# Kernel tuning notes

Measured on AMD Instinct MI355X. Metric: run time of the kernel, lower is better.

The kernel has to match this reference:

```python
import jax, jax.numpy as jnp
import numpy as np

HIDDEN = 2048
N_HEADS = 32
N_KV_HEADS = 8
HEAD_DIM = 64
MAX_SEQ_LEN = 4096
ROPE_THETA = 500000.0
B, L = 1, 2048
EPS = 1e-6
NEG = -1e9


def precompute_rope(head_dim, max_seq_len, theta):
    freqs = 1.0 / theta ** (jnp.arange(0, head_dim, 2, dtype=jnp.float32) / head_dim)
    pos = jnp.arange(max_seq_len, dtype=jnp.float32)
    ang = pos[:, None] * freqs[None, :]                     # [S, hd/2]
    cos = jnp.repeat(jnp.cos(ang), 2, axis=-1)              # [S, hd]
    sin = jnp.repeat(jnp.sin(ang), 2, axis=-1)
    return cos, sin


def apply_rope(x, cos, sin):
    # x: [B, H, L, hd]; interleaved (even/odd) rotation, faithful to torch code
    seq_len = x.shape[2]
    c = cos[:seq_len][None, None, :, ::2]                   # [1,1,L,hd/2]
    s = sin[:seq_len][None, None, :, ::2]
    x1 = x[..., ::2]
    x2 = x[..., 1::2]
    o1 = x1 * c - x2 * s
    o2 = x2 * c + x1 * s
    return jnp.stack([o1, o2], axis=-1).reshape(x.shape)


def rmsnorm(x, w):
    return x * jax.lax.rsqrt(jnp.mean(x * x, axis=-1, keepdims=True) + EPS) * w


def setup_inputs() -> dict:
    key = jax.random.key(0)
    ks = jax.random.split(key, 6)
    x = jax.random.normal(ks[0], (B, L, HIDDEN), dtype=jnp.float32)
    causal = jnp.tril(jnp.ones((L, L), dtype=bool))
    mask = jnp.where(causal, 0.0, NEG).astype(jnp.float32)  # additive causal mask
    scale = 0.02
    norm_w = jnp.ones((HIDDEN,), dtype=jnp.float32)
    Wq = jax.random.normal(ks[1], (N_HEADS * HEAD_DIM, HIDDEN), dtype=jnp.float32) * scale
    Wk = jax.random.normal(ks[2], (N_KV_HEADS * HEAD_DIM, HIDDEN), dtype=jnp.float32) * scale
    Wv = jax.random.normal(ks[3], (N_KV_HEADS * HEAD_DIM, HIDDEN), dtype=jnp.float32) * scale
    Wo = jax.random.normal(ks[4], (HIDDEN, N_HEADS * HEAD_DIM), dtype=jnp.float32) * scale
    rope_cos, rope_sin = precompute_rope(HEAD_DIM, MAX_SEQ_LEN, ROPE_THETA)
    return {"x": x, "mask": mask, "norm_w": norm_w, "Wq": Wq, "Wk": Wk,
            "Wv": Wv, "Wo": Wo, "rope_cos": rope_cos, "rope_sin": rope_sin}


def reference(x, mask, norm_w, Wq, Wk, Wv, Wo, rope_cos, rope_sin):
    Bb, Ll, _ = x.shape
    residual = x
    h = rmsnorm(x, norm_w)
    q = (h @ Wq.T).reshape(Bb, Ll, N_HEADS, HEAD_DIM).transpose(0, 2, 1, 3)     # [B,H,L,hd]
    k = (h @ Wk.T).reshape(Bb, Ll, N_KV_HEADS, HEAD_DIM).transpose(0, 2, 1, 3)  # [B,Hk,L,hd]
    v = (h @ Wv.T).reshape(Bb, Ll, N_KV_HEADS, HEAD_DIM).transpose(0, 2, 1, 3)
    q = apply_rope(q, rope_cos, rope_sin)
    k = apply_rope(k, rope_cos, rope_sin)
    n_groups = N_HEADS // N_KV_HEADS
    if n_groups > 1:
        k = jnp.repeat(k, n_groups, axis=1)   # GQA repeat_interleave
        v = jnp.repeat(v, n_groups, axis=1)
    scale = jnp.sqrt(jnp.asarray(HEAD_DIM, dtype=q.dtype))
    attn = jnp.einsum('bhld,bhmd->bhlm', q, k) / scale
    attn = attn + mask                                       # broadcast [L,L]
    attn = jax.nn.softmax(attn, axis=-1)
    out = jnp.einsum('bhlm,bhmd->bhld', attn, v)
    out = out.transpose(0, 2, 1, 3).reshape(Bb, Ll, N_HEADS * HEAD_DIM)
    return out @ Wo.T + residual
```

## Files before the change

kernel.cpp:

```cpp
#include <hip/hip_runtime.h>
#include <stdint.h>

#define L_SEQ 2048
#define HID   2048
#define NHEAD 32
#define NKV   8
#define HD    64
#define KVDIM 512
#define QSCALE 0.18033688f

typedef __attribute__((ext_vector_type(8))) short s16x8;
typedef __attribute__((ext_vector_type(4))) short s16x4;
typedef __attribute__((ext_vector_type(4))) float f32x4;

__device__ __forceinline__ short f2bf(float f) {
  __bf16 b = (__bf16)f;
  short s;
  __builtin_memcpy(&s, &b, 2);
  return s;
}

__device__ __forceinline__ void gload16(const void* g, void* l) {
  __builtin_amdgcn_global_load_lds(
      (const __attribute__((address_space(1))) void*)g,
      (__attribute__((address_space(3))) void*)l, 16, 0, 0);
}

__global__ __launch_bounds__(256) void pre_kernel(
    const float* __restrict__ x, const float* __restrict__ w,
    const float* __restrict__ wq, const float* __restrict__ wk,
    const float* __restrict__ wv, const float* __restrict__ wo,
    short* __restrict__ h,
    short* __restrict__ owq, short* __restrict__ owk,
    short* __restrict__ owv, short* __restrict__ owo) {
  const int tid = threadIdx.x;
  if (blockIdx.x >= 2048) {
    int64_t e = ((int64_t)(blockIdx.x - 2048) * 256 + tid) * 4;
    const float* src; short* dst; int64_t o;
    if (e < 4194304)      { src = wq; dst = owq; o = e; }
    else if (e < 5242880) { src = wk; dst = owk; o = e - 4194304; }
    else if (e < 6291456) { src = wv; dst = owv; o = e - 5242880; }
    else                  { src = wo; dst = owo; o = e - 6291456; }
    f32x4 v = *(const f32x4*)(src + o);
    s16x4 b;
    b[0] = f2bf(v[0]); b[1] = f2bf(v[1]); b[2] = f2bf(v[2]); b[3] = f2bf(v[3]);
    *(s16x4*)(dst + o) = b;
    return;
  }
  const int row = blockIdx.x;
  const float* xr = x + (int64_t)row * HID + tid * 8;
  f32x4 a = *(const f32x4*)(xr);
  f32x4 b = *(const f32x4*)(xr + 4);
  float ss = a[0]*a[0]+a[1]*a[1]+a[2]*a[2]+a[3]*a[3]
           + b[0]*b[0]+b[1]*b[1]+b[2]*b[2]+b[3]*b[3];
  #pragma unroll
  for (int off = 1; off < 64; off <<= 1) ss += __shfl_xor(ss, off, 64);
  __shared__ float sred[4];
  if ((tid & 63) == 0) sred[tid >> 6] = ss;
  __syncthreads();
  const float scale = rsqrtf((sred[0]+sred[1]+sred[2]+sred[3]) * (1.0f/HID) + 1e-6f);
  const float* wp = w + tid * 8;
  f32x4 wa = *(const f32x4*)(wp);
  f32x4 wb = *(const f32x4*)(wp + 4);
  s16x8 o;
  o[0]=f2bf(a[0]*scale*wa[0]); o[1]=f2bf(a[1]*scale*wa[1]);
  o[2]=f2bf(a[2]*scale*wa[2]); o[3]=f2bf(a[3]*scale*wa[3]);
  o[4]=f2bf(b[0]*scale*wb[0]); o[5]=f2bf(b[1]*scale*wb[1]);
  o[6]=f2bf(b[2]*scale*wb[2]); o[7]=f2bf(b[3]*scale*wb[3]);
  *(s16x8*)(h + (int64_t)row * HID + tid * 8) = o;
}

__device__ __forceinline__ void gemm_core_128x64(
    const short* __restrict__ A, const short* __restrict__ B,
    short* sA, short* sB, f32x4 acc[4][2]) {
  const int tid = threadIdx.x;
  const int lane = tid & 63;
  const int w = tid >> 6, wr = w >> 1, wc = w & 1;
  const int g = lane >> 4, li = lane & 15;

  auto stage = [&](int k0, int buf) {
    #pragma unroll
    for (int i = 0; i < 4; ++i) {
      const int flat = i * 256 + tid;
      const int row = flat >> 3, c8 = flat & 7;
      const int sc = c8 ^ (row & 7);
      gload16(A + (int64_t)row * HID + k0 + sc * 8, sA + buf * 8192 + flat * 8);
    }
    #pragma unroll
    for (int i = 0; i < 2; ++i) {
      const int flat = i * 256 + tid;
      const int row = flat >> 3, c8 = flat & 7;
      const int sc = c8 ^ (row & 7);
      gload16(B + (int64_t)row * HID + k0 + sc * 8, sB + buf * 4096 + flat * 8);
    }
  };

  stage(0, 0);
  for (int k0 = 0; k0 < HID; k0 += 64) {
    const int cur = (k0 >> 6) & 1;
    __syncthreads();
    if (k0 + 64 < HID) stage(k0 + 64, cur ^ 1);
    const short* cA = sA + cur * 8192;
    const short* cB = sB + cur * 4096;
    #pragma unroll
    for (int kk = 0; kk < 2; ++kk) {
      s16x8 af[4], bfr[2];
      const int chunk = (kk << 2) | g;
      #pragma unroll
      for (int m = 0; m < 4; ++m) {
        const int row = wr * 64 + m * 16 + li;
        af[m] = *(const s16x8*)(cA + row * 64 + ((chunk ^ (li & 7)) << 3));
      }
      #pragma unroll
      for (int n = 0; n < 2; ++n) {
        const int row = wc * 32 + n * 16 + li;
        bfr[n] = *(const s16x8*)(cB + row * 64 + ((chunk ^ (li & 7)) << 3));
      }
      __builtin_amdgcn_s_setprio(1);
      #pragma unroll
      for (int m = 0; m < 4; ++m)
        #pragma unroll
        for (int n = 0; n < 2; ++n)
          acc[m][n] = __builtin_amdgcn_mfma_f32_16x16x32_bf16(af[m], bfr[n], acc[m][n], 0, 0, 0);
      __builtin_amdgcn_s_setprio(0);
    }
  }
}

__global__ __launch_bounds__(256) void qkv_kernel(
    const short* __restrict__ h16, const short* __restrict__ wq,
    const short* __restrict__ wk, const short* __restrict__ wv,
    short* __restrict__ qo, short* __restrict__ ko, short* __restrict__ vto,
    const float* __restrict__ rc, const float* __restrict__ rs) {
  __shared__ short sA[2 * 128 * 64];
  __shared__ short sB[2 * 64 * 64];
  const int cb = blockIdx.x, rb = blockIdx.y;
  const short* B; short* out; int colbase, mode; int64_t ldc;
  if (cb < 32)      { B = wq + (int64_t)cb * 64 * HID;        out = qo;  colbase = cb * 64;        mode = 0; ldc = HID;   }
  else if (cb < 40) { B = wk + (int64_t)(cb - 32) * 64 * HID; out = ko;  colbase = (cb - 32) * 64; mode = 0; ldc = KVDIM; }
  else              { B = wv + (int64_t)(cb - 40) * 64 * HID; out = vto; colbase = (cb - 40) * 64; mode = 1; ldc = L_SEQ; }
  const float rsc = (cb < 32) ? QSCALE : 1.0f;

  f32x4 acc[4][2];
  const f32x4 z = {0.f, 0.f, 0.f, 0.f};
  #pragma unroll
  for (int m = 0; m < 4; ++m)
    #pragma unroll
    for (int n = 0; n < 2; ++n) acc[m][n] = z;

  gemm_core_128x64(h16 + (int64_t)rb * 128 * HID, B, sA, sB, acc);

  const int lane = threadIdx.x & 63;
  const int w = threadIdx.x >> 6, wr = w >> 1, wc = w & 1;
  const int g = lane >> 4, li = lane & 15;

  if (mode == 0) {
    #pragma unroll
    for (int m = 0; m < 4; ++m) {
      #pragma unroll
      for (int n = 0; n < 2; ++n) {
        const int col = colbase + wc * 32 + n * 16 + li;
        const int d2 = col & 62;
        #pragma unroll
        for (int r = 0; r < 4; ++r) {
          const int row = rb * 128 + wr * 64 + m * 16 + g * 4 + r;
          const float c = rc[row * 64 + d2] * rsc;
          const float s = rs[row * 64 + d2] * rsc;
          const float v0 = acc[m][n][r];
          const float pr = __shfl_xor(v0, 1, 64);
          const float o = (lane & 1) ? (v0 * c + pr * s) : (v0 * c - pr * s);
          out[(int64_t)row * ldc + col] = f2bf(o);
        }
      }
    }
  } else {
    #pragma unroll
    for (int m = 0; m < 4; ++m) {
      #pragma unroll
      for (int n = 0; n < 2; ++n) {
        const int col = colbase + wc * 32 + n * 16 + li;
        const int row0 = rb * 128 + wr * 64 + m * 16 + g * 4;
        s16x4 pk;
        pk[0] = f2bf(acc[m][n][0]); pk[1] = f2bf(acc[m][n][1]);
        pk[2] = f2bf(acc[m][n][2]); pk[3] = f2bf(acc[m][n][3]);
        *(s16x4*)(out + (int64_t)col * L_SEQ + row0) = pk;
      }
    }
  }
}

__global__ __launch_bounds__(512, 4) void attn_kernel(
    const short* __restrict__ q16, const short* __restrict__ k16,
    const short* __restrict__ vt16, short* __restrict__ out16) {
  __shared__ short sK[4 * 64 * 64];
  __shared__ short sV[4 * 64 * 64];
  __shared__ short sP[8][16 * 64];
  const int pi = blockIdx.x, h = blockIdx.y, kvh = h >> 2;
  const int qbL = pi, qbH = 31 - pi;
  const int tid = threadIdx.x, lane = tid & 63, w = tid >> 6, wl = w & 3;
  const int g = lane >> 4, li = lane & 15;
  const int myqb = (w < 4) ? qbL : qbH;
  short* sPw = &sP[w][0];

  s16x8 qf[2];
  {
    const int qr = myqb * 64 + wl * 16 + li;
    #pragma unroll
    for (int kk = 0; kk < 2; ++kk)
      qf[kk] = *(const s16x8*)(q16 + (int64_t)qr * HID + h * 64 + kk * 32 + g * 8);
  }

  f32x4 acc[4];
  const f32x4 z = {0.f, 0.f, 0.f, 0.f};
  #pragma unroll
  for (int n = 0; n < 4; ++n) acc[n] = z;
  float m = -1e30f, l = 0.f;

  auto stage1 = [&](int t, int buf, int slot) {
    const int kv0 = t * 64;
    const int row = tid >> 3, c8 = tid & 7;
    const int sc = c8 ^ (row & 7);
    const int off = (buf * 2 + slot) * 4096;
    gload16(k16 + (int64_t)(kv0 + row) * KVDIM + kvh * 64 + sc * 8,
            sK + off + tid * 8);
    gload16(vt16 + (int64_t)(kvh * 64 + row) * L_SEQ + kv0 + sc * 8,
            sV + off + tid * 8);
  };

  stage1(0, 0, 0);
  stage1(1, 0, 1);
  for (int tp = 0; 2 * tp <= qbH; ++tp) {
    const int buf = tp & 1;
    __syncthreads();
    if (2 * tp + 2 <= qbH) {
      stage1(2 * tp + 2, buf ^ 1, 0);
      const int t3 = 2 * tp + 3;
      stage1(t3 <= qbH ? t3 : t3 - 1, buf ^ 1, 1);
    }
    #pragma unroll
    for (int sl = 0; sl < 2; ++sl) {
      const int t = 2 * tp + sl;
      if (t <= qbH && (w >= 4 || t <= qbL)) {
        const short* cK = sK + (buf * 2 + sl) * 4096;
        const short* cV = sV + (buf * 2 + sl) * 4096;

        s16x8 kf[2][4];
        #pragma unroll
        for (int kk = 0; kk < 2; ++kk)
          #pragma unroll
          for (int n = 0; n < 4; ++n)
            kf[kk][n] = *(const s16x8*)(cK + (n * 16 + li) * 64 + ((((kk << 2) | g) ^ (li & 7)) << 3));
        f32x4 s[4];
        #pragma unroll
        for (int n = 0; n < 4; ++n) s[n] = z;
        __builtin_amdgcn_s_setprio(1);
        #pragma unroll
        for (int kk = 0; kk < 2; ++kk)
          #pragma unroll
          for (int n = 0; n < 4; ++n)
            s[n] = __builtin_amdgcn_mfma_f32_16x16x32_bf16(kf[kk][n], qf[kk], s[n], 0, 0, 0);
        __builtin_amdgcn_s_setprio(0);

        s16x8 vf[2][4];
        #pragma unroll
        for (int kk = 0; kk < 2; ++kk)
          #pragma unroll
          for (int dt = 0; dt < 4; ++dt)
            vf[kk][dt] = *(const s16x8*)(cV + (dt * 16 + li) * 64 + ((((kk << 2) | g) ^ (li & 7)) << 3));

        if (t == myqb) {
          const int ql = wl * 16 + li;
          #pragma unroll
          for (int n = 0; n < 4; ++n)
            #pragma unroll
            for (int r = 0; r < 4; ++r)
              if (n * 16 + g * 4 + r > ql) s[n][r] = -1e30f;
        }

        float mx = fmaxf(fmaxf(s[0][0], s[0][1]), fmaxf(s[0][2], s[0][3]));
        #pragma unroll
        for (int n = 1; n < 4; ++n)
          mx = fmaxf(mx, fmaxf(fmaxf(s[n][0], s[n][1]), fmaxf(s[n][2], s[n][3])));
        mx = fmaxf(mx, __shfl_xor(mx, 16, 64));
        mx = fmaxf(mx, __shfl_xor(mx, 32, 64));
        if (__any(mx > m + 8.0f)) {
          const float mn = fmaxf(m, mx);
          const float al = __builtin_amdgcn_exp2f(m - mn);
          m = mn;
          l *= al;
          #pragma unroll
          for (int dt = 0; dt < 4; ++dt)
            #pragma unroll
            for (int r = 0; r < 4; ++r) acc[dt][r] *= al;
        }
        float ps = 0.f;
        #pragma unroll
        for (int n = 0; n < 4; ++n) {
          s16x4 pk;
          #pragma unroll
          for (int r = 0; r < 4; ++r) {
            const float p = __builtin_amdgcn_exp2f(s[n][r] - m);
            pk[r] = f2bf(p);
            ps += p;
          }
          *(s16x4*)(sPw + li * 64 + (((n * 2 + (g >> 1)) ^ (li & 7)) << 3) + (g & 1) * 4) = pk;
        }
        ps += __shfl_xor(ps, 16, 64);
        ps += __shfl_xor(ps, 32, 64);
        l += ps;

        #pragma unroll
        for (int kk = 0; kk < 2; ++kk) {
          s16x8 pf = *(const s16x8*)(sPw + li * 64 + (((kk * 4 + g) ^ (li & 7)) << 3));
          __builtin_amdgcn_s_setprio(1);
          #pragma unroll
          for (int dt = 0; dt < 4; ++dt)
            acc[dt] = __builtin_amdgcn_mfma_f32_16x16x32_bf16(vf[kk][dt], pf, acc[dt], 0, 0, 0);
          __builtin_amdgcn_s_setprio(0);
        }
      }
    }
  }

  const float rl = 1.0f / l;
  #pragma unroll
  for (int n2 = 0; n2 < 4; ++n2) {
    s16x4 o;
    #pragma unroll
    for (int r = 0; r < 4; ++r) o[r] = f2bf(acc[n2][r] * rl);
    *(s16x4*)(sPw + li * 64 + (((n2 * 2 + (g >> 1)) ^ (li & 7)) << 3) + (g & 1) * 4) = o;
  }
  #pragma unroll
  for (int half = 0; half < 2; ++half) {
    const int chunk = half * 64 + lane;
    const int q = chunk >> 3, c = chunk & 7;
    s16x8 v = *(const s16x8*)(sPw + q * 64 + ((c ^ (q & 7)) << 3));
    *(s16x8*)(out16 + (int64_t)(myqb * 64 + wl * 16 + q) * HID + h * 64 + c * 8) = v;
  }
}

__global__ __launch_bounds__(256) void oproj_kernel(
    const short* __restrict__ ao, const short* __restrict__ wo,
    const float* __restrict__ resid, float* __restrict__ out) {
  __shared__ short sA[2 * 128 * 64];
  __shared__ short sB[2 * 64 * 64];
  const int cb = blockIdx.x, rb = blockIdx.y;
  f32x4 acc[4][2];
  const f32x4 z = {0.f, 0.f, 0.f, 0.f};
  #pragma unroll
  for (int m = 0; m < 4; ++m)
    #pragma unroll
    for (int n = 0; n < 2; ++n) acc[m][n] = z;

  gemm_core_128x64(ao + (int64_t)rb * 128 * HID, wo + (int64_t)cb * 64 * HID, sA, sB, acc);

  const int lane = threadIdx.x & 63;
  const int w = threadIdx.x >> 6, wr = w >> 1, wc = w & 1;
  const int g = lane >> 4, li = lane & 15;
  #pragma unroll
  for (int m = 0; m < 4; ++m) {
    #pragma unroll
    for (int n = 0; n < 2; ++n) {
      const int col = cb * 64 + wc * 32 + n * 16 + li;
      #pragma unroll
      for (int r = 0; r < 4; ++r) {
        const int row = rb * 128 + wr * 64 + m * 16 + g * 4 + r;
        out[(int64_t)row * HID + col] = acc[m][n][r] + resid[(int64_t)row * HID + col];
      }
    }
  }
}

extern "C" void kernel_launch(void* const* d_in, const int* in_sizes, int n_in,
                              void* d_out, int out_size, void* d_ws, size_t ws_size,
                              hipStream_t stream) {
  (void)in_sizes; (void)n_in; (void)out_size; (void)ws_size;
  const float* x      = (const float*)d_in[0];
  const float* norm_w = (const float*)d_in[2];
  const float* Wq     = (const float*)d_in[3];
  const float* Wk     = (const float*)d_in[4];
  const float* Wv     = (const float*)d_in[5];
  const float* Wo     = (const float*)d_in[6];
  const float* rc     = (const float*)d_in[7];
  const float* rs     = (const float*)d_in[8];
  float* out = (float*)d_out;

  char* ws = (char*)d_ws;
  short* wq16 = (short*)(ws);
  short* wk16 = (short*)(ws + 8388608);
  short* wv16 = (short*)(ws + 10485760);
  short* wo16 = (short*)(ws + 12582912);
  short* h16  = (short*)(ws + 20971520);
  short* q16  = (short*)(ws + 29360128);
  short* k16  = (short*)(ws + 37748736);
  short* vt16 = (short*)(ws + 39845888);
  short* ao16 = (short*)(ws + 41943040);

  pre_kernel<<<12288, 256, 0, stream>>>(x, norm_w, Wq, Wk, Wv, Wo,
                                        h16, wq16, wk16, wv16, wo16);
  qkv_kernel<<<dim3(48, 16), 256, 0, stream>>>(h16, wq16, wk16, wv16, q16, k16, vt16, rc, rs);
  attn_kernel<<<dim3(16, NHEAD), 512, 0, stream>>>(q16, k16, vt16, ao16);
  oproj_kernel<<<dim3(32, 16), 256, 0, stream>>>(ao16, wo16, x, out);
}
```

Baseline: 123.8 us.

## Process two KV tiles per online-softmax step in attention loop

Restructures the flash-attention inner loop so both KV tiles staged per iteration are scored together and share a single max/rescale and row-sum reduction. This halves the online-softmax bookkeeping (shuffles, rescale checks) per tile. V fragments are loaded just before use to cut register pressure, and the global-load pointers become incrementing pointers instead of being recomputed from the tile index. The risk is more live registers for the two score tiles, which could lower occupancy.

```diff
diff --git a/kernel.cpp b/kernel.cpp
--- a/kernel.cpp
+++ b/kernel.cpp
@@ -216,110 +216,164 @@
   for (int n = 0; n < 4; ++n) acc[n] = z;
   float m = -1e30f, l = 0.f;
 
-  auto stage1 = [&](int t, int buf, int slot) {
-    const int kv0 = t * 64;
-    const int row = tid >> 3, c8 = tid & 7;
-    const int sc = c8 ^ (row & 7);
+  const int srow = tid >> 3, sc8 = tid & 7;
+  const int ssc = sc8 ^ (srow & 7);
+  const short* kp = k16 + (int64_t)srow * KVDIM + kvh * 64 + ssc * 8;
+  const short* vp = vt16 + (int64_t)(kvh * 64 + srow) * L_SEQ + ssc * 8;
+  auto stage1 = [&](int buf, int slot) {
     const int off = (buf * 2 + slot) * 4096;
-    gload16(k16 + (int64_t)(kv0 + row) * KVDIM + kvh * 64 + sc * 8,
-            sK + off + tid * 8);
-    gload16(vt16 + (int64_t)(kvh * 64 + row) * L_SEQ + kv0 + sc * 8,
-            sV + off + tid * 8);
+    gload16(kp, sK + off + tid * 8);
+    gload16(vp, sV + off + tid * 8);
+    kp += 64 * KVDIM;
+    vp += 64;
   };
 
-  stage1(0, 0, 0);
-  stage1(1, 0, 1);
+  stage1(0, 0);
+  stage1(0, 1);
   for (int tp = 0; 2 * tp <= qbH; ++tp) {
     const int buf = tp & 1;
     __syncthreads();
     if (2 * tp + 2 <= qbH) {
-      stage1(2 * tp + 2, buf ^ 1, 0);
-      const int t3 = 2 * tp + 3;
-      stage1(t3 <= qbH ? t3 : t3 - 1, buf ^ 1, 1);
-    }
-    #pragma unroll
-    for (int sl = 0; sl < 2; ++sl) {
-      const int t = 2 * tp + sl;
-      if (t <= qbH && (w >= 4 || t <= qbL)) {
-        const short* cK = sK + (buf * 2 + sl) * 4096;
-        const short* cV = sV + (buf * 2 + sl) * 4096;
-
-        s16x8 kf[2][4];
-        #pragma unroll
-        for (int kk = 0; kk < 2; ++kk)
-          #pragma unroll
-          for (int n = 0; n < 4; ++n)
-            kf[kk][n] = *(const s16x8*)(cK + (n * 16 + li) * 64 + ((((kk << 2) | g) ^ (li & 7)) << 3));
-        f32x4 s[4];
-        #pragma unroll
-        for (int n = 0; n < 4; ++n) s[n] = z;
+      stage1(buf ^ 1, 0);
+      stage1(buf ^ 1, 1);
+    }
+    const int t0 = 2 * tp, t1 = t0 + 1;
+    const bool a0 = (t0 <= myqb);
+    const bool a1 = (t1 <= myqb);
+    if (!a0) continue;
+    const short* cK0 = sK + (buf * 2 + 0) * 4096;
+    const short* cV0 = sV + (buf * 2 + 0) * 4096;
+    const short* cK1 = sK + (buf * 2 + 1) * 4096;
+    const short* cV1 = sV + (buf * 2 + 1) * 4096;
+
+    f32x4 s0[4], s1[4];
+    {
+      s16x8 kf[2][4];
+      #pragma unroll
+      for (int kk = 0; kk < 2; ++kk)
+        #pragma unroll
+        for (int n = 0; n < 4; ++n)
+          kf[kk][n] = *(const s16x8*)(cK0 + (n * 16 + li) * 64 + ((((kk << 2) | g) ^ (li & 7)) << 3));
+      #pragma unroll
+      for (int n = 0; n < 4; ++n) s0[n] = z;
+      __builtin_amdgcn_s_setprio(1);
+      #pragma unroll
+      for (int kk = 0; kk < 2; ++kk)
+        #pragma unroll
+        for (int n = 0; n < 4; ++n)
+          s0[n] = __builtin_amdgcn_mfma_f32_16x16x32_bf16(kf[kk][n], qf[kk], s0[n], 0, 0, 0);
+      __builtin_amdgcn_s_setprio(0);
+    }
+    if (a1) {
+      s16x8 kf[2][4];
+      #pragma unroll
+      for (int kk = 0; kk < 2; ++kk)
+        #pragma unroll
+        for (int n = 0; n < 4; ++n)
+          kf[kk][n] = *(const s16x8*)(cK1 + (n * 16 + li) * 64 + ((((kk << 2) | g) ^ (li & 7)) << 3));
+      #pragma unroll
+      for (int n = 0; n < 4; ++n) s1[n] = z;
+      __builtin_amdgcn_s_setprio(1);
+      #pragma unroll
+      for (int kk = 0; kk < 2; ++kk)
+        #pragma unroll
+        for (int n = 0; n < 4; ++n)
+          s1[n] = __builtin_amdgcn_mfma_f32_16x16x32_bf16(kf[kk][n], qf[kk], s1[n], 0, 0, 0);
+      __builtin_amdgcn_s_setprio(0);
+    }
+
+    if (t0 == myqb) {
+      const int ql = wl * 16 + li;
+      #pragma unroll
+      for (int n = 0; n < 4; ++n)
+        #pragma unroll
+        for (int r = 0; r < 4; ++r)
+          if (n * 16 + g * 4 + r > ql) s0[n][r] = -1e30f;
+    }
+    if (a1 && t1 == myqb) {
+      const int ql = wl * 16 + li;
+      #pragma unroll
+      for (int n = 0; n < 4; ++n)
+        #pragma unroll
+        for (int r = 0; r < 4; ++r)
+          if (n * 16 + g * 4 + r > ql) s1[n][r] = -1e30f;
+    }
+
+    float mx = fmaxf(fmaxf(s0[0][0], s0[0][1]), fmaxf(s0[0][2], s0[0][3]));
+    #pragma unroll
+    for (int n = 1; n < 4; ++n)
+      mx = fmaxf(mx, fmaxf(fmaxf(s0[n][0], s0[n][1]), fmaxf(s0[n][2], s0[n][3])));
+    if (a1)
+      #pragma unroll
+      for (int n = 0; n < 4; ++n)
+        mx = fmaxf(mx, fmaxf(fmaxf(s1[n][0], s1[n][1]), fmaxf(s1[n][2], s1[n][3])));
+    mx = fmaxf(mx, __shfl_xor(mx, 16, 64));
+    mx = fmaxf(mx, __shfl_xor(mx, 32, 64));
+    if (__any(mx > m + 8.0f)) {
+      const float mn = fmaxf(m, mx);
+      const float al = __builtin_amdgcn_exp2f(m - mn);
+      m = mn;
+      l *= al;
+      #pragma unroll
+      for (int dt = 0; dt < 4; ++dt)
+        #pragma unroll
+        for (int r = 0; r < 4; ++r) acc[dt][r] *= al;
+    }
+
+    float ps = 0.f;
+    #pragma unroll
+    for (int n = 0; n < 4; ++n) {
+      s16x4 pk;
+      #pragma unroll
+      for (int r = 0; r < 4; ++r) {
+        const float p = __builtin_amdgcn_exp2f(s0[n][r] - m);
+        pk[r] = f2bf(p);
+        ps += p;
+      }
+      *(s16x4*)(sPw + li * 64 + (((n * 2 + (g >> 1)) ^ (li & 7)) << 3) + (g & 1) * 4) = pk;
+    }
+    #pragma unroll
+    for (int kk = 0; kk < 2; ++kk) {
+      s16x8 vf[4];
+      #pragma unroll
+      for (int dt = 0; dt < 4; ++dt)
+        vf[dt] = *(const s16x8*)(cV0 + (dt * 16 + li) * 64 + ((((kk << 2) | g) ^ (li & 7)) << 3));
+      s16x8 pf = *(const s16x8*)(sPw + li * 64 + (((kk * 4 + g) ^ (li & 7)) << 3));
+      __builtin_amdgcn_s_setprio(1);
+      #pragma unroll
+      for (int dt = 0; dt < 4; ++dt)
+        acc[dt] = __builtin_amdgcn_mfma_f32_16x16x32_bf16(vf[dt], pf, acc[dt], 0, 0, 0);
+      __builtin_amdgcn_s_setprio(0);
+    }
+    if (a1) {
+      #pragma unroll
+      for (int n = 0; n < 4; ++n) {
+        s16x4 pk;
+        #pragma unroll
+        for (int r = 0; r < 4; ++r) {
+          const float p = __builtin_amdgcn_exp2f(s1[n][r] - m);
+          pk[r] = f2bf(p);
+          ps += p;
+        }
+        *(s16x4*)(sPw + li * 64 + (((n * 2 + (g >> 1)) ^ (li & 7)) << 3) + (g & 1) * 4) = pk;
+      }
+      #pragma unroll
+      for (int kk = 0; kk < 2; ++kk) {
+        s16x8 vf[4];
+        #pragma unroll
+        for (int dt = 0; dt < 4; ++dt)
+          vf[dt] = *(const s16x8*)(cV1 + (dt * 16 + li) * 64 + ((((kk << 2) | g) ^ (li & 7)) << 3));
+        s16x8 pf = *(const s16x8*)(sPw + li * 64 + (((kk * 4 + g) ^ (li & 7)) << 3));
         __builtin_amdgcn_s_setprio(1);
         #pragma unroll
-        for (int kk = 0; kk < 2; ++kk)
-          #pragma unroll
-          for (int n = 0; n < 4; ++n)
-            s[n] = __builtin_amdgcn_mfma_f32_16x16x32_bf16(kf[kk][n], qf[kk], s[n], 0, 0, 0);
+        for (int dt = 0; dt < 4; ++dt)
+          acc[dt] = __builtin_amdgcn_mfma_f32_16x16x32_bf16(vf[dt], pf, acc[dt], 0, 0, 0);
         __builtin_amdgcn_s_setprio(0);
-
-        s16x8 vf[2][4];
-        #pragma unroll
-        for (int kk = 0; kk < 2; ++kk)
-          #pragma unroll
-          for (int dt = 0; dt < 4; ++dt)
-            vf[kk][dt] = *(const s16x8*)(cV + (dt * 16 + li) * 64 + ((((kk << 2) | g) ^ (li & 7)) << 3));
-
-        if (t == myqb) {
-          const int ql = wl * 16 + li;
-          #pragma unroll
-          for (int n = 0; n < 4; ++n)
-            #pragma unroll
-            for (int r = 0; r < 4; ++r)
-              if (n * 16 + g * 4 + r > ql) s[n][r] = -1e30f;
-        }
-
-        float mx = fmaxf(fmaxf(s[0][0], s[0][1]), fmaxf(s[0][2], s[0][3]));
-        #pragma unroll
-        for (int n = 1; n < 4; ++n)
-          mx = fmaxf(mx, fmaxf(fmaxf(s[n][0], s[n][1]), fmaxf(s[n][2], s[n][3])));
-        mx = fmaxf(mx, __shfl_xor(mx, 16, 64));
-        mx = fmaxf(mx, __shfl_xor(mx, 32, 64));
-        if (__any(mx > m + 8.0f)) {
-          const float mn = fmaxf(m, mx);
-          const float al = __builtin_amdgcn_exp2f(m - mn);
-          m = mn;
-          l *= al;
-          #pragma unroll
-          for (int dt = 0; dt < 4; ++dt)
-            #pragma unroll
-            for (int r = 0; r < 4; ++r) acc[dt][r] *= al;
-        }
-        float ps = 0.f;
-        #pragma unroll
-        for (int n = 0; n < 4; ++n) {
-          s16x4 pk;
-          #pragma unroll
-          for (int r = 0; r < 4; ++r) {
-            const float p = __builtin_amdgcn_exp2f(s[n][r] - m);
-            pk[r] = f2bf(p);
-            ps += p;
-          }
-          *(s16x4*)(sPw + li * 64 + (((n * 2 + (g >> 1)) ^ (li & 7)) << 3) + (g & 1) * 4) = pk;
-        }
-        ps += __shfl_xor(ps, 16, 64);
-        ps += __shfl_xor(ps, 32, 64);
-        l += ps;
-
-        #pragma unroll
-        for (int kk = 0; kk < 2; ++kk) {
-          s16x8 pf = *(const s16x8*)(sPw + li * 64 + (((kk * 4 + g) ^ (li & 7)) << 3));
-          __builtin_amdgcn_s_setprio(1);
-          #pragma unroll
-          for (int dt = 0; dt < 4; ++dt)
-            acc[dt] = __builtin_amdgcn_mfma_f32_16x16x32_bf16(vf[kk][dt], pf, acc[dt], 0, 0, 0);
-          __builtin_amdgcn_s_setprio(0);
-        }
-      }
-    }
+      }
+    }
+    ps += __shfl_xor(ps, 16, 64);
+    ps += __shfl_xor(ps, 32, 64);
+    l += ps;
   }
 
   const float rl = 1.0f / l;
```

Result: no change. 121.4 us (-2.0%).

## Give each attention wave two 16-row query tiles and process KV tiles in pairs

Applied to the files above, without the earlier changes.

The attention block drops from 8 waves to 4, and each wave now owns 32 query rows as two 16-row tiles. Every K/V fragment read from shared memory feeds two MFMAs, which halves LDS read traffic per unit of work. The softmax max and rescale are now done once per pair of KV tiles instead of per tile. Staging uses precomputed pointers that are advanced each step. The cost is more registers per wave and fewer waves to hide latency, with launch bounds changed to 256 threads at 2 blocks.

```diff
diff --git a/kernel.cpp b/kernel.cpp
--- a/kernel.cpp
+++ b/kernel.cpp
@@ -189,154 +189,211 @@
   }
 }
 
-__global__ __launch_bounds__(512, 4) void attn_kernel(
+__global__ __launch_bounds__(256, 2) void attn_kernel(
     const short* __restrict__ q16, const short* __restrict__ k16,
     const short* __restrict__ vt16, short* __restrict__ out16) {
   __shared__ short sK[4 * 64 * 64];
   __shared__ short sV[4 * 64 * 64];
-  __shared__ short sP[8][16 * 64];
+  __shared__ short sP[4][2][16 * 64];
   const int pi = blockIdx.x, h = blockIdx.y, kvh = h >> 2;
   const int qbL = pi, qbH = 31 - pi;
-  const int tid = threadIdx.x, lane = tid & 63, w = tid >> 6, wl = w & 3;
+  const int tid = threadIdx.x, lane = tid & 63, w = tid >> 6;
   const int g = lane >> 4, li = lane & 15;
-  const int myqb = (w < 4) ? qbL : qbH;
-  short* sPw = &sP[w][0];
-
-  s16x8 qf[2];
+  const int myqb = (w < 2) ? qbL : qbH;
+  const int rbase = (w & 1) * 32;
+  short* sPwA = &sP[w][0][0];
+  short* sPwB = &sP[w][1][0];
+
+  s16x8 qfA[2], qfB[2];
   {
-    const int qr = myqb * 64 + wl * 16 + li;
-    #pragma unroll
-    for (int kk = 0; kk < 2; ++kk)
-      qf[kk] = *(const s16x8*)(q16 + (int64_t)qr * HID + h * 64 + kk * 32 + g * 8);
-  }
-
-  f32x4 acc[4];
+    const int qrA = myqb * 64 + rbase + li;
+    #pragma unroll
+    for (int kk = 0; kk < 2; ++kk) {
+      qfA[kk] = *(const s16x8*)(q16 + (int64_t)qrA * HID + h * 64 + kk * 32 + g * 8);
+      qfB[kk] = *(const s16x8*)(q16 + (int64_t)(qrA + 16) * HID + h * 64 + kk * 32 + g * 8);
+    }
+  }
+
+  f32x4 accA[4], accB[4];
   const f32x4 z = {0.f, 0.f, 0.f, 0.f};
   #pragma unroll
-  for (int n = 0; n < 4; ++n) acc[n] = z;
-  float m = -1e30f, l = 0.f;
-
-  auto stage1 = [&](int t, int buf, int slot) {
-    const int kv0 = t * 64;
-    const int row = tid >> 3, c8 = tid & 7;
-    const int sc = c8 ^ (row & 7);
+  for (int n = 0; n < 4; ++n) { accA[n] = z; accB[n] = z; }
+  float mA = -1e30f, lA = 0.f, mB = -1e30f, lB = 0.f;
+
+  const int srow = tid >> 3, sc8 = tid & 7;
+  const int ssc = sc8 ^ (srow & 7);
+  const short* kp0 = k16 + (int64_t)srow * KVDIM + kvh * 64 + ssc * 8;
+  const short* kp1 = kp0 + 32 * KVDIM;
+  const short* vp0 = vt16 + (int64_t)(kvh * 64 + srow) * L_SEQ + ssc * 8;
+  const short* vp1 = vp0 + 32 * L_SEQ;
+  auto stage1 = [&](int buf, int slot) {
     const int off = (buf * 2 + slot) * 4096;
-    gload16(k16 + (int64_t)(kv0 + row) * KVDIM + kvh * 64 + sc * 8,
-            sK + off + tid * 8);
-    gload16(vt16 + (int64_t)(kvh * 64 + row) * L_SEQ + kv0 + sc * 8,
-            sV + off + tid * 8);
-  };
-
-  stage1(0, 0, 0);
-  stage1(1, 0, 1);
+    gload16(kp0, sK + off + tid * 8);
+    gload16(kp1, sK + off + 2048 + tid * 8);
+    gload16(vp0, sV + off + tid * 8);
+    gload16(vp1, sV + off + 2048 + tid * 8);
+    kp0 += 64 * KVDIM; kp1 += 64 * KVDIM;
+    vp0 += 64; vp1 += 64;
+  };
+
+  auto qk2 = [&](const short* cK, f32x4 sa[4], f32x4 sb[4]) {
+    s16x8 kf[2][4];
+    #pragma unroll
+    for (int kk = 0; kk < 2; ++kk)
+      #pragma unroll
+      for (int n = 0; n < 4; ++n)
+        kf[kk][n] = *(const s16x8*)(cK + (n * 16 + li) * 64 + ((((kk << 2) | g) ^ (li & 7)) << 3));
+    #pragma unroll
+    for (int n = 0; n < 4; ++n) { sa[n] = z; sb[n] = z; }
+    __builtin_amdgcn_s_setprio(1);
+    #pragma unroll
+    for (int kk = 0; kk < 2; ++kk)
+      #pragma unroll
+      for (int n = 0; n < 4; ++n) {
+        sa[n] = __builtin_amdgcn_mfma_f32_16x16x32_bf16(kf[kk][n], qfA[kk], sa[n], 0, 0, 0);
+        sb[n] = __builtin_amdgcn_mfma_f32_16x16x32_bf16(kf[kk][n], qfB[kk], sb[n], 0, 0, 0);
+      }
+    __builtin_amdgcn_s_setprio(0);
+  };
+
+  auto maskdiag = [&](f32x4 s[4], int ql) {
+    #pragma unroll
+    for (int n = 0; n < 4; ++n)
+      #pragma unroll
+      for (int r = 0; r < 4; ++r)
+        if (n * 16 + g * 4 + r > ql) s[n][r] = -1e30f;
+  };
+
+  auto packP = [&](const f32x4 s[4], float mm, float& ps, short* sPw) {
+    #pragma unroll
+    for (int n = 0; n < 4; ++n) {
+      s16x4 pk;
+      #pragma unroll
+      for (int r = 0; r < 4; ++r) {
+        const float p = __builtin_amdgcn_exp2f(s[n][r] - mm);
+        pk[r] = f2bf(p);
+        ps += p;
+      }
+      *(s16x4*)(sPw + li * 64 + (((n * 2 + (g >> 1)) ^ (li & 7)) << 3) + (g & 1) * 4) = pk;
+    }
+  };
+
+  auto pv2 = [&]( const short* cV) {
+    #pragma unroll
+    for (int kk = 0; kk < 2; ++kk) {
+      s16x8 vf[4];
+      #pragma unroll
+      for (int dt = 0; dt < 4; ++dt)
+        vf[dt] = *(const s16x8*)(cV + (dt * 16 + li) * 64 + ((((kk << 2) | g) ^ (li & 7)) << 3));
+      s16x8 pfA = *(const s16x8*)(sPwA + li * 64 + (((kk * 4 + g) ^ (li & 7)) << 3));
+      s16x8 pfB = *(const s16x8*)(sPwB + li * 64 + (((kk * 4 + g) ^ (li & 7)) << 3));
+      __builtin_amdgcn_s_setprio(1);
+      #pragma unroll
+      for (int dt = 0; dt < 4; ++dt) {
+        accA[dt] = __builtin_amdgcn_mfma_f32_16x16x32_bf16(vf[dt], pfA, accA[dt], 0, 0, 0);
+        accB[dt] = __builtin_amdgcn_mfma_f32_16x16x32_bf16(vf[dt], pfB, accB[dt], 0, 0, 0);
+      }
+      __builtin_amdgcn_s_setprio(0);
+    }
+  };
+
+  stage1(0, 0);
+  stage1(0, 1);
   for (int tp = 0; 2 * tp <= qbH; ++tp) {
     const int buf = tp & 1;
     __syncthreads();
     if (2 * tp + 2 <= qbH) {
-      stage1(2 * tp + 2, buf ^ 1, 0);
-      const int t3 = 2 * tp + 3;
-      stage1(t3 <= qbH ? t3 : t3 - 1, buf ^ 1, 1);
-    }
-    #pragma unroll
-    for (int sl = 0; sl < 2; ++sl) {
-      const int t = 2 * tp + sl;
-      if (t <= qbH && (w >= 4 || t <= qbL)) {
-        const short* cK = sK + (buf * 2 + sl) * 4096;
-        const short* cV = sV + (buf * 2 + sl) * 4096;
-
-        s16x8 kf[2][4];
+      stage1(buf ^ 1, 0);
+      stage1(buf ^ 1, 1);
+    }
+    const int t0 = 2 * tp, t1 = t0 + 1;
+    const bool a0 = (t0 <= myqb);
+    const bool a1 = (t1 <= myqb);
+    if (!a0) continue;
+    const short* cK0 = sK + (buf * 2 + 0) * 4096;
+    const short* cV0 = sV + (buf * 2 + 0) * 4096;
+    const short* cK1 = sK + (buf * 2 + 1) * 4096;
+    const short* cV1 = sV + (buf * 2 + 1) * 4096;
+
+    f32x4 sA0[4], sB0[4], sA1[4], sB1[4];
+    qk2(cK0, sA0, sB0);
+    if (a1) qk2(cK1, sA1, sB1);
+
+    if (t0 == myqb) { maskdiag(sA0, rbase + li); maskdiag(sB0, rbase + 16 + li); }
+    if (a1 && t1 == myqb) { maskdiag(sA1, rbase + li); maskdiag(sB1, rbase + 16 + li); }
+
+    float mxA = fmaxf(fmaxf(sA0[0][0], sA0[0][1]), fmaxf(sA0[0][2], sA0[0][3]));
+    float mxB = fmaxf(fmaxf(sB0[0][0], sB0[0][1]), fmaxf(sB0[0][2], sB0[0][3]));
+    #pragma unroll
+    for (int n = 1; n < 4; ++n) {
+      mxA = fmaxf(mxA, fmaxf(fmaxf(sA0[n][0], sA0[n][1]), fmaxf(sA0[n][2], sA0[n][3])));
+      mxB = fmaxf(mxB, fmaxf(fmaxf(sB0[n][0], sB0[n][1]), fmaxf(sB0[n][2], sB0[n][3])));
+    }
+    if (a1)
+      #pragma unroll
+      for (int n = 0; n < 4; ++n) {
+        mxA = fmaxf(mxA, fmaxf(fmaxf(sA1[n][0], sA1[n][1]), fmaxf(sA1[n][2], sA1[n][3])));
+        mxB = fmaxf(mxB, fmaxf(fmaxf(sB1[n][0], sB1[n][1]), fmaxf(sB1[n][2], sB1[n][3])));
+      }
+    mxA = fmaxf(mxA, __shfl_xor(mxA, 16, 64));
+    mxA = fmaxf(mxA, __shfl_xor(mxA, 32, 64));
+    mxB = fmaxf(mxB, __shfl_xor(mxB, 16, 64));
+    mxB = fmaxf(mxB, __shfl_xor(mxB, 32, 64));
+    if (__any(mxA > mA + 8.0f)) {
+      const float mn = fmaxf(mA, mxA);
+      const float al = __builtin_amdgcn_exp2f(mA - mn);
+      mA = mn; lA *= al;
+      #pragma unroll
+      for (int dt = 0; dt < 4; ++dt)
         #pragma unroll
-        for (int kk = 0; kk < 2; ++kk)
-          #pragma unroll
-          for (int n = 0; n < 4; ++n)
-            kf[kk][n] = *(const s16x8*)(cK + (n * 16 + li) * 64 + ((((kk << 2) | g) ^ (li & 7)) << 3));
-        f32x4 s[4];
+        for (int r = 0; r < 4; ++r) accA[dt][r] *= al;
+    }
+    if (__any(mxB > mB + 8.0f)) {
+      const float mn = fmaxf(mB, mxB);
+      const float al = __builtin_amdgcn_exp2f(mB - mn);
+      mB = mn; lB *= al;
+      #pragma unroll
+      for (int dt = 0; dt < 4; ++dt)
         #pragma unroll
-        for (int n = 0; n < 4; ++n) s[n] = z;
-        __builtin_amdgcn_s_setprio(1);
-        #pragma unroll
-        for (int kk = 0; kk < 2; ++kk)
-          #pragma unroll
-          for (int n = 0; n < 4; ++n)
-            s[n] = __builtin_amdgcn_mfma_f32_16x16x32_bf16(kf[kk][n], qf[kk], s[n], 0, 0, 0);
-        __builtin_amdgcn_s_setprio(0);
-
-        s16x8 vf[2][4];
-        #pragma unroll
-        for (int kk = 0; kk < 2; ++kk)
-          #pragma unroll
-          for (int dt = 0; dt < 4; ++dt)
-            vf[kk][dt] = *(const s16x8*)(cV + (dt * 16 + li) * 64 + ((((kk << 2) | g) ^ (li & 7)) << 3));
-
-        if (t == myqb) {
-          const int ql = wl * 16 + li;
-          #pragma unroll
-          for (int n = 0; n < 4; ++n)
-            #pragma unroll
-            for (int r = 0; r < 4; ++r)
-              if (n * 16 + g * 4 + r > ql) s[n][r] = -1e30f;
-        }
-
-        float mx = fmaxf(fmaxf(s[0][0], s[0][1]), fmaxf(s[0][2], s[0][3]));
-        #pragma unroll
-        for (int n = 1; n < 4; ++n)
-          mx = fmaxf(mx, fmaxf(fmaxf(s[n][0], s[n][1]), fmaxf(s[n][2], s[n][3])));
-        mx = fmaxf(mx, __shfl_xor(mx, 16, 64));
-        mx = fmaxf(mx, __shfl_xor(mx, 32, 64));
-        if (__any(mx > m + 8.0f)) {
-          const float mn = fmaxf(m, mx);
-          const float al = __builtin_amdgcn_exp2f(m - mn);
-          m = mn;
-          l *= al;
-          #pragma unroll
-          for (int dt = 0; dt < 4; ++dt)
-            #pragma unroll
-            for (int r = 0; r < 4; ++r) acc[dt][r] *= al;
-        }
-        float ps = 0.f;
-        #pragma unroll
-        for (int n = 0; n < 4; ++n) {
-          s16x4 pk;
-          #pragma unroll
-          for (int r = 0; r < 4; ++r) {
-            const float p = __builtin_amdgcn_exp2f(s[n][r] - m);
-            pk[r] = f2bf(p);
-            ps += p;
-          }
-          *(s16x4*)(sPw + li * 64 + (((n * 2 + (g >> 1)) ^ (li & 7)) << 3) + (g & 1) * 4) = pk;
-        }
-        ps += __shfl_xor(ps, 16, 64);
-        ps += __shfl_xor(ps, 32, 64);
-        l += ps;
-
-        #pragma unroll
-        for (int kk = 0; kk < 2; ++kk) {
-          s16x8 pf = *(const s16x8*)(sPw + li * 64 + (((kk * 4 + g) ^ (li & 7)) << 3));
-          __builtin_amdgcn_s_setprio(1);
-          #pragma unroll
-          for (int dt = 0; dt < 4; ++dt)
-            acc[dt] = __builtin_amdgcn_mfma_f32_16x16x32_bf16(vf[kk][dt], pf, acc[dt], 0, 0, 0);
-          __builtin_amdgcn_s_setprio(0);
-        }
-      }
-    }
-  }
-
-  const float rl = 1.0f / l;
-  #pragma unroll
-  for (int n2 = 0; n2 < 4; ++n2) {
-    s16x4 o;
-    #pragma unroll
-    for (int r = 0; r < 4; ++r) o[r] = f2bf(acc[n2][r] * rl);
-    *(s16x4*)(sPw + li * 64 + (((n2 * 2 + (g >> 1)) ^ (li & 7)) << 3) + (g & 1) * 4) = o;
-  }
-  #pragma unroll
-  for (int half = 0; half < 2; ++half) {
-    const int chunk = half * 64 + lane;
-    const int q = chunk >> 3, c = chunk & 7;
-    s16x8 v = *(const s16x8*)(sPw + q * 64 + ((c ^ (q & 7)) << 3));
-    *(s16x8*)(out16 + (int64_t)(myqb * 64 + wl * 16 + q) * HID + h * 64 + c * 8) = v;
-  }
+        for (int r = 0; r < 4; ++r) accB[dt][r] *= al;
+    }
+
+    float psA = 0.f, psB = 0.f;
+    packP(sA0, mA, psA, sPwA);
+    packP(sB0, mB, psB, sPwB);
+    pv2(cV0);
+    if (a1) {
+      packP(sA1, mA, psA, sPwA);
+      packP(sB1, mB, psB, sPwB);
+      pv2(cV1);
+    }
+    psA += __shfl_xor(psA, 16, 64);
+    psA += __shfl_xor(psA, 32, 64);
+    psB += __shfl_xor(psB, 16, 64);
+    psB += __shfl_xor(psB, 32, 64);
+    lA += psA;
+    lB += psB;
+  }
+
+  auto wout = [&](const f32x4 acc[4], float l, int rb2, short* sPw) {
+    const float rl = 1.0f / l;
+    #pragma unroll
+    for (int n2 = 0; n2 < 4; ++n2) {
+      s16x4 o;
+      #pragma unroll
+      for (int r = 0; r < 4; ++r) o[r] = f2bf(acc[n2][r] * rl);
+      *(s16x4*)(sPw + li * 64 + (((n2 * 2 + (g >> 1)) ^ (li & 7)) << 3) + (g & 1) * 4) = o;
+    }
+    #pragma unroll
+    for (int half = 0; half < 2; ++half) {
+      const int chunk = half * 64 + lane;
+      const int q = chunk >> 3, c = chunk & 7;
+      s16x8 v = *(const s16x8*)(sPw + q * 64 + ((c ^ (q & 7)) << 3));
+      *(s16x8*)(out16 + (int64_t)(myqb * 64 + rb2 + q) * HID + h * 64 + c * 8) = v;
+    }
+  };
+  wout(accA, lA, rbase, sPwA);
+  wout(accB, lB, rbase + 16, sPwB);
 }
 
 __global__ __launch_bounds__(256) void oproj_kernel(
@@ -399,6 +456,6 @@
   pre_kernel<<<12288, 256, 0, stream>>>(x, norm_w, Wq, Wk, Wv, Wo,
                                         h16, wq16, wk16, wv16, wo16);
   qkv_kernel<<<dim3(48, 16), 256, 0, stream>>>(h16, wq16, wk16, wv16, q16, k16, vt16, rc, rs);
-  attn_kernel<<<dim3(16, NHEAD), 512, 0, stream>>>(q16, k16, vt16, ao16);
+  attn_kernel<<<dim3(16, NHEAD), 256, 0, stream>>>(q16, k16, vt16, ao16);
   oproj_kernel<<<dim3(32, 16), 256, 0, stream>>>(ao16, wo16, x, out);
 }
```

New measurement: 133.8 us. 8.0% more time.
